# Kernel optimization log

Measured on AMD Instinct MI355X. Metric: run time of the kernel, lower is better.

## Reference

```python
import jax, jax.numpy as jnp
import numpy as np

WIN = 7
K1, K2 = 0.01, 0.03
NP_ = WIN ** 3
COV_NORM = NP_ / (NP_ - 1)


def _box3d(x, win=WIN):
    # Separable box filter: three 1D VALID convs (same math as the dense
    for ax in range(3):
        kshape = [1, 1, 1, 1, 1]
        kshape[2 + ax] = win
        k = jnp.ones(kshape, x.dtype) / win
        x = jax.lax.conv_general_dilated(
            x, k, window_strides=(1, 1, 1), padding='VALID',
            dimension_numbers=('NCDHW', 'OIDHW', 'NCDHW'))
    return x


def setup_inputs() -> dict:
    key = jax.random.key(0)
    k1, k2 = jax.random.split(key)
    B, C, D, H, W = 4, 1, 128, 128, 128
    X = jax.random.normal(k1, (B, C, D, H, W), dtype=jnp.float32)
    Y = jax.random.normal(k2, (B, C, D, H, W), dtype=jnp.float32)
    data_range = jnp.ones((B, 1, 1, 1, 1), dtype=jnp.float32)
    return {"X": X, "Y": Y, "data_range": data_range}


def reference(X, Y, data_range):
    C1 = (K1 * data_range) ** 2
    C2 = (K2 * data_range) ** 2
    ux = _box3d(X)
    uy = _box3d(Y)
    uxx = _box3d(X * X)
    uyy = _box3d(Y * Y)
    uxy = _box3d(X * Y)
    vx = COV_NORM * (uxx - ux * ux)
    vy = COV_NORM * (uyy - uy * uy)
    vxy = COV_NORM * (uxy - ux * uy)
    A1 = 2 * ux * uy + C1
    A2 = 2 * vxy + C2
    B1 = ux ** 2 + uy ** 2 + C1
    B2 = vx + vy + C2
    S = (A1 * A2) / (B1 * B2)
    return S.mean()
```

## Files before the change

### kernel.cpp

```cpp
#include <hip/hip_runtime.h>

#define NFULL 128
#define NOUT  122
#define NBLK  768

#define WROW 34
#define WQ   748
#define WB   3740
#define HROW 34
#define HQ   544
#define HB   2720

__device__ __forceinline__ void phaseA_task(const float* __restrict__ px,
                                            const float* __restrict__ py,
                                            float* __restrict__ wp)
{
    float xs[8], ys[8];
#pragma unroll
    for (int k = 0; k < 4; ++k) {
        float2 tx = *(const float2*)(px + 2 * k);
        float2 ty = *(const float2*)(py + 2 * k);
        xs[2 * k] = tx.x; xs[2 * k + 1] = tx.y;
        ys[2 * k] = ty.x; ys[2 * k + 1] = ty.y;
    }
    float sx = 0.f, sy = 0.f, sxx = 0.f, syy = 0.f, sxy = 0.f;
#pragma unroll
    for (int k = 0; k < 7; ++k) {
        sx += xs[k]; sy += ys[k];
        sxx = fmaf(xs[k], xs[k], sxx);
        syy = fmaf(ys[k], ys[k], syy);
        sxy = fmaf(xs[k], ys[k], sxy);
    }
    float tx2 = sx - xs[0] + xs[7];
    float ty2 = sy - ys[0] + ys[7];
    float txx = sxx - xs[0] * xs[0] + xs[7] * xs[7];
    float tyy = syy - ys[0] * ys[0] + ys[7] * ys[7];
    float txy = sxy - xs[0] * ys[0] + xs[7] * ys[7];
    *(float2*)(wp + 0 * WQ) = make_float2(sx,  tx2);
    *(float2*)(wp + 1 * WQ) = make_float2(sy,  ty2);
    *(float2*)(wp + 2 * WQ) = make_float2(sxx, txx);
    *(float2*)(wp + 3 * WQ) = make_float2(syy, tyy);
    *(float2*)(wp + 4 * WQ) = make_float2(sxy, txy);
}

__global__ __launch_bounds__(256, 3)
void ssim3d_kernel(const float* __restrict__ X, const float* __restrict__ Y,
                   const float* __restrict__ DR, double* __restrict__ ws,
                   float* __restrict__ out, int mode)
{
    __shared__ __align__(16) float wbuf[2 * WB];
    __shared__ __align__(16) float hbuf[2 * HB];
    __shared__ float  redf[4];
    __shared__ double redd[4];
    __shared__ int lastFlag;

    const int tid = threadIdx.x;
    int bi = blockIdx.x;
    const int bb = bi & 3;  bi >>= 2;
    const int ht = bi & 7;  bi >>= 3;
    const int wt = bi & 3;  bi >>= 2;
    const int dc = bi;

    const int h0 = ht << 4;
    const int w0 = (wt == 3) ? 90 : (wt << 5);
    const int w_hi = (wt == 3) ? 122 : ((wt == 2) ? 90 : (w0 + 32));
    const int csize = (dc < 2) ? 21 : 20;
    const int d0 = (dc < 2) ? dc * 21 : 42 + (dc - 2) * 20;
    const int nsl = csize + 6;

    const float dr = DR[bb];
    const float c1s = (0.01f * dr) * (0.01f * dr) * 117649.0f;
    const float c2s = (0.03f * dr) * (0.03f * dr) * 117649.0f;
    const float tni = 1.0f / 343.0f;
    const float kkA = 2.0f * 117649.0f / 342.0f;
    const float kkB = 117649.0f / 342.0f;

    const int sA  = tid & 15;
    const int rA0 = tid >> 4;
    int grA0 = h0 + rA0; if (grA0 > NFULL - 1) grA0 = NFULL - 1;
    const int coffA = w0 + 2 * sA;
    const int eA = tid - 192;
    int rA1 = 0, cA1 = 0, grA1 = 0, rA2 = 0, cA2 = 0, grA2 = 0;
    if (eA >= 0) {
        rA1 = 16 + (eA >> 4); cA1 = eA & 15;
        grA1 = h0 + rA1; if (grA1 > NFULL - 1) grA1 = NFULL - 1;
        if (eA < 32) {
            const int t = eA + 64;
            rA2 = 16 + (t >> 4); cA2 = t & 15;
            grA2 = h0 + rA2; if (grA2 > NFULL - 1) grA2 = NFULL - 1;
        }
    }

    const int bq = tid >> 5;
    const int bc = tid & 31;

    const int sC = tid & 15, hC = tid >> 4;
    const int gh  = h0 + hC;
    const int gw0 = w0 + 2 * sC;
    const bool vh = (gh < NOUT);
    const bool vld0 = vh && (gw0 < w_hi);
    const bool vld1 = vh && (gw0 + 1 < w_hi);

    const size_t planeStride = (size_t)NFULL * NFULL;
    const size_t bbase = (size_t)bb * NFULL * planeStride;

    float2 ring[7][5];
    float2 run[5];
#pragma unroll
    for (int k = 0; k < 7; ++k)
#pragma unroll
        for (int q = 0; q < 5; ++q) ring[k][q] = make_float2(0.f, 0.f);
#pragma unroll
    for (int q = 0; q < 5; ++q) run[q] = make_float2(0.f, 0.f);
    float acc = 0.0f;

    for (int base = 0; base <= nsl + 1; base += 7) {
#pragma unroll
        for (int u = 0; u < 7; ++u) {
            const int s = base + u;
            if (s <= nsl + 1) {
                if (s < nsl) {
                    float* dst = wbuf + (size_t)((s & 1) * WB);
                    const int dIn = d0 + s;
                    const float* Xp = X + bbase + (size_t)dIn * planeStride;
                    const float* Yp = Y + bbase + (size_t)dIn * planeStride;
                    phaseA_task(Xp + grA0 * NFULL + coffA, Yp + grA0 * NFULL + coffA,
                                dst + rA0 * WROW + 2 * sA);
                    if (eA >= 0) {
                        const int co1 = w0 + 2 * cA1;
                        phaseA_task(Xp + grA1 * NFULL + co1, Yp + grA1 * NFULL + co1,
                                    dst + rA1 * WROW + 2 * cA1);
                        if (eA < 32) {
                            const int co2 = w0 + 2 * cA2;
                            phaseA_task(Xp + grA2 * NFULL + co2, Yp + grA2 * NFULL + co2,
                                        dst + rA2 * WROW + 2 * cA2);
                        }
                    }
                }
                if (s >= 1 && tid < 160) {
                    const float* src = wbuf + (size_t)(((s - 1) & 1) * WB) + bq * WQ + bc;
                    float* dst = hbuf + (size_t)(((s - 1) & 1) * HB) + bq * HQ + bc;
                    float win = src[0] + src[WROW] + src[2 * WROW] + src[3 * WROW]
                              + src[4 * WROW] + src[5 * WROW];
#pragma unroll
                    for (int h = 0; h < 16; ++h) {
                        win += src[(h + 6) * WROW];
                        dst[h * HROW] = win;
                        win -= src[h * WROW];
                    }
                }
                if (s >= 2) {
                    const float* src = hbuf + (size_t)((s & 1) * HB) + hC * HROW + 2 * sC;
                    const int slot = (u + 5) % 7;
#pragma unroll
                    for (int q = 0; q < 5; ++q) {
                        float2 h2 = *(const float2*)(src + q * HQ);
                        run[q].x += h2.x - ring[slot][q].x;
                        run[q].y += h2.y - ring[slot][q].y;
                        ring[slot][q] = h2;
                    }
                    if (s >= 8) {
#pragma unroll
                        for (int j = 0; j < 2; ++j) {
                            const bool vld = j ? vld1 : vld0;
                            if (vld) {
                                float Sx  = j ? run[0].y : run[0].x;
                                float Sy  = j ? run[1].y : run[1].x;
                                float Sxx = j ? run[2].y : run[2].x;
                                float Syy = j ? run[3].y : run[3].x;
                                float Sxy = j ? run[4].y : run[4].x;
                                float P = Sx * Sy;
                                float Q = fmaf(Sx, Sx, Sy * Sy);
                                float A1 = fmaf(2.f, P, c1s);
                                float A2 = fmaf(kkA, fmaf(-tni, P, Sxy), c2s);
                                float B1 = Q + c1s;
                                float B2 = fmaf(kkB, fmaf(-tni, Q, Sxx + Syy), c2s);
                                float num = A1 * A2;
                                float den = B1 * B2;
                                float r0 = __builtin_amdgcn_rcpf(den);
                                r0 = r0 * fmaf(-den, r0, 2.0f);
                                acc = fmaf(num, r0, acc);
                            }
                        }
                    }
                }
                __syncthreads();
            }
        }
    }

#pragma unroll
    for (int off = 32; off; off >>= 1) acc += __shfl_down(acc, off);
    if ((tid & 63) == 0) redf[tid >> 6] = acc;
    __syncthreads();

    if (mode) {
        if (tid == 0) {
            double t = (double)redf[0] + (double)redf[1] + (double)redf[2] + (double)redf[3];
            ws[blockIdx.x] = t;
            __threadfence();
            unsigned int old = atomicAdd((unsigned int*)(ws + NBLK), 1u);
            lastFlag = (old == NBLK - 1) ? 1 : 0;
        }
        __syncthreads();
        if (lastFlag) {
            __threadfence();
            double t = 0.0;
            for (int i = tid; i < NBLK; i += 256) t += ws[i];
#pragma unroll
            for (int off = 32; off; off >>= 1) t += __shfl_down(t, off);
            if ((tid & 63) == 0) redd[tid >> 6] = t;
            __syncthreads();
            if (tid == 0)
                out[0] = (float)((redd[0] + redd[1] + redd[2] + redd[3])
                                 * (1.0 / 7263392.0));
        }
    } else {
        if (tid == 0) {
            double t = (double)redf[0] + (double)redf[1] + (double)redf[2] + (double)redf[3];
            atomicAdd(ws, t);
        }
    }
}

__global__ void ssim3d_finalize(const double* __restrict__ ws, float* __restrict__ out)
{
    out[0] = (float)(ws[0] * (1.0 / 7263392.0));
}

extern "C" void kernel_launch(void* const* d_in, const int* in_sizes, int n_in,
                              void* d_out, int out_size, void* d_ws, size_t ws_size,
                              hipStream_t stream)
{
    const float* X  = (const float*)d_in[0];
    const float* Y  = (const float*)d_in[1];
    const float* DR = (const float*)d_in[2];
    double* ws = (double*)d_ws;

    const int mode = (ws_size >= (size_t)(NBLK + 1) * sizeof(double)) ? 1 : 0;
    if (mode)
        hipMemsetAsync((char*)d_ws + (size_t)NBLK * sizeof(double), 0, sizeof(double), stream);
    else
        hipMemsetAsync(d_ws, 0, sizeof(double), stream);

    ssim3d_kernel<<<NBLK, 256, 0, stream>>>(X, Y, DR, ws, (float*)d_out, mode);
    if (!mode) ssim3d_finalize<<<1, 1, 0, stream>>>(ws, (float*)d_out);
}
```

Before: 146.3 us.

## Use 512-thread blocks with specialized warps and single-buffered staging

Blocks grow to 512 threads and the grid shrinks to 512 blocks, with larger depth chunks (30-31 slices) so each block re-reads fewer halo slices. Threads 160+ now load and do the W-pass while all threads do a one-pixel-per-thread depth ring and SSIM evaluation. Double buffering is replaced by single buffers with two barriers per slice. The aim is to cut halo reloads and raise parallelism, at the cost of more synchronization and a serialized H-pass phase.

```diff
diff --git a/kernel.cpp b/kernel.cpp
--- a/kernel.cpp
+++ b/kernel.cpp
@@ -2,7 +2,8 @@
 
 #define NFULL 128
 #define NOUT  122
-#define NBLK  768
+#define NBLK  512
+#define NTHR  512
 
 #define WROW 34
 #define WQ   748
@@ -43,15 +44,15 @@
     *(float2*)(wp + 4 * WQ) = make_float2(sxy, txy);
 }
 
-__global__ __launch_bounds__(256, 3)
+__global__ __launch_bounds__(NTHR, 4)
 void ssim3d_kernel(const float* __restrict__ X, const float* __restrict__ Y,
                    const float* __restrict__ DR, double* __restrict__ ws,
                    float* __restrict__ out, int mode)
 {
-    __shared__ __align__(16) float wbuf[2 * WB];
-    __shared__ __align__(16) float hbuf[2 * HB];
-    __shared__ float  redf[4];
-    __shared__ double redd[4];
+    __shared__ __align__(16) float wbuf[WB];
+    __shared__ __align__(16) float hbuf[HB];
+    __shared__ float  redf[8];
+    __shared__ double redd[8];
     __shared__ int lastFlag;
 
     const int tid = threadIdx.x;
@@ -64,8 +65,8 @@
     const int h0 = ht << 4;
     const int w0 = (wt == 3) ? 90 : (wt << 5);
     const int w_hi = (wt == 3) ? 122 : ((wt == 2) ? 90 : (w0 + 32));
-    const int csize = (dc < 2) ? 21 : 20;
-    const int d0 = (dc < 2) ? dc * 21 : 42 + (dc - 2) * 20;
+    const int csize = (dc < 2) ? 31 : 30;
+    const int d0 = (dc < 2) ? dc * 31 : 62 + (dc - 2) * 30;
     const int nsl = csize + 6;
 
     const float dr = DR[bb];
@@ -75,113 +76,84 @@
     const float kkA = 2.0f * 117649.0f / 342.0f;
     const float kkB = 117649.0f / 342.0f;
 
-    const int sA  = tid & 15;
-    const int rA0 = tid >> 4;
-    int grA0 = h0 + rA0; if (grA0 > NFULL - 1) grA0 = NFULL - 1;
+    const int aid = tid - 160;
+    const int rA  = aid >> 4;
+    const int sA  = aid & 15;
+    int grA = h0 + rA; if (grA > NFULL - 1) grA = NFULL - 1;
     const int coffA = w0 + 2 * sA;
-    const int eA = tid - 192;
-    int rA1 = 0, cA1 = 0, grA1 = 0, rA2 = 0, cA2 = 0, grA2 = 0;
-    if (eA >= 0) {
-        rA1 = 16 + (eA >> 4); cA1 = eA & 15;
-        grA1 = h0 + rA1; if (grA1 > NFULL - 1) grA1 = NFULL - 1;
-        if (eA < 32) {
-            const int t = eA + 64;
-            rA2 = 16 + (t >> 4); cA2 = t & 15;
-            grA2 = h0 + rA2; if (grA2 > NFULL - 1) grA2 = NFULL - 1;
-        }
-    }
 
     const int bq = tid >> 5;
     const int bc = tid & 31;
 
-    const int sC = tid & 15, hC = tid >> 4;
-    const int gh  = h0 + hC;
-    const int gw0 = w0 + 2 * sC;
-    const bool vh = (gh < NOUT);
-    const bool vld0 = vh && (gw0 < w_hi);
-    const bool vld1 = vh && (gw0 + 1 < w_hi);
+    const int sC = tid & 31, hC = tid >> 5;
+    const int gh = h0 + hC;
+    const int gw = w0 + sC;
+    const bool vld = (gh < NOUT) && (gw < w_hi);
 
     const size_t planeStride = (size_t)NFULL * NFULL;
     const size_t bbase = (size_t)bb * NFULL * planeStride;
 
-    float2 ring[7][5];
-    float2 run[5];
+    float ring[7][5];
+    float run[5];
 #pragma unroll
     for (int k = 0; k < 7; ++k)
 #pragma unroll
-        for (int q = 0; q < 5; ++q) ring[k][q] = make_float2(0.f, 0.f);
-#pragma unroll
-    for (int q = 0; q < 5; ++q) run[q] = make_float2(0.f, 0.f);
+        for (int q = 0; q < 5; ++q) ring[k][q] = 0.f;
+#pragma unroll
+    for (int q = 0; q < 5; ++q) run[q] = 0.f;
     float acc = 0.0f;
 
-    for (int base = 0; base <= nsl + 1; base += 7) {
+    for (int base = 0; base <= nsl; base += 7) {
 #pragma unroll
         for (int u = 0; u < 7; ++u) {
             const int s = base + u;
-            if (s <= nsl + 1) {
-                if (s < nsl) {
-                    float* dst = wbuf + (size_t)((s & 1) * WB);
+            if (s <= nsl) {
+                if (s < nsl && aid >= 0) {
                     const int dIn = d0 + s;
                     const float* Xp = X + bbase + (size_t)dIn * planeStride;
                     const float* Yp = Y + bbase + (size_t)dIn * planeStride;
-                    phaseA_task(Xp + grA0 * NFULL + coffA, Yp + grA0 * NFULL + coffA,
-                                dst + rA0 * WROW + 2 * sA);
-                    if (eA >= 0) {
-                        const int co1 = w0 + 2 * cA1;
-                        phaseA_task(Xp + grA1 * NFULL + co1, Yp + grA1 * NFULL + co1,
-                                    dst + rA1 * WROW + 2 * cA1);
-                        if (eA < 32) {
-                            const int co2 = w0 + 2 * cA2;
-                            phaseA_task(Xp + grA2 * NFULL + co2, Yp + grA2 * NFULL + co2,
-                                        dst + rA2 * WROW + 2 * cA2);
-                        }
+                    phaseA_task(Xp + grA * NFULL + coffA, Yp + grA * NFULL + coffA,
+                                wbuf + rA * WROW + 2 * sA);
+                }
+                if (s >= 1) {
+                    const float* src = hbuf + hC * HROW + sC;
+                    const int slot = (u + 6) % 7;
+#pragma unroll
+                    for (int q = 0; q < 5; ++q) {
+                        float v = src[q * HQ];
+                        run[q] += v - ring[slot][q];
+                        ring[slot][q] = v;
+                    }
+                    if (s >= 7 && vld) {
+                        float Sx  = run[0];
+                        float Sy  = run[1];
+                        float Sxx = run[2];
+                        float Syy = run[3];
+                        float Sxy = run[4];
+                        float P = Sx * Sy;
+                        float Q = fmaf(Sx, Sx, Sy * Sy);
+                        float A1 = fmaf(2.f, P, c1s);
+                        float A2 = fmaf(kkA, fmaf(-tni, P, Sxy), c2s);
+                        float B1 = Q + c1s;
+                        float B2 = fmaf(kkB, fmaf(-tni, Q, Sxx + Syy), c2s);
+                        float num = A1 * A2;
+                        float den = B1 * B2;
+                        float r0 = __builtin_amdgcn_rcpf(den);
+                        r0 = r0 * fmaf(-den, r0, 2.0f);
+                        acc = fmaf(num, r0, acc);
                     }
                 }
-                if (s >= 1 && tid < 160) {
-                    const float* src = wbuf + (size_t)(((s - 1) & 1) * WB) + bq * WQ + bc;
-                    float* dst = hbuf + (size_t)(((s - 1) & 1) * HB) + bq * HQ + bc;
-                    float win = src[0] + src[WROW] + src[2 * WROW] + src[3 * WROW]
-                              + src[4 * WROW] + src[5 * WROW];
+                __syncthreads();
+                if (s < nsl && tid < 160) {
+                    const float* srcw = wbuf + bq * WQ + bc;
+                    float* dsth = hbuf + bq * HQ + bc;
+                    float win = srcw[0] + srcw[WROW] + srcw[2 * WROW]
+                              + srcw[3 * WROW] + srcw[4 * WROW] + srcw[5 * WROW];
 #pragma unroll
                     for (int h = 0; h < 16; ++h) {
-                        win += src[(h + 6) * WROW];
-                        dst[h * HROW] = win;
-                        win -= src[h * WROW];
-                    }
-                }
-                if (s >= 2) {
-                    const float* src = hbuf + (size_t)((s & 1) * HB) + hC * HROW + 2 * sC;
-                    const int slot = (u + 5) % 7;
-#pragma unroll
-                    for (int q = 0; q < 5; ++q) {
-                        float2 h2 = *(const float2*)(src + q * HQ);
-                        run[q].x += h2.x - ring[slot][q].x;
-                        run[q].y += h2.y - ring[slot][q].y;
-                        ring[slot][q] = h2;
-                    }
-                    if (s >= 8) {
-#pragma unroll
-                        for (int j = 0; j < 2; ++j) {
-                            const bool vld = j ? vld1 : vld0;
-                            if (vld) {
-                                float Sx  = j ? run[0].y : run[0].x;
-                                float Sy  = j ? run[1].y : run[1].x;
-                                float Sxx = j ? run[2].y : run[2].x;
-                                float Syy = j ? run[3].y : run[3].x;
-                                float Sxy = j ? run[4].y : run[4].x;
-                                float P = Sx * Sy;
-                                float Q = fmaf(Sx, Sx, Sy * Sy);
-                                float A1 = fmaf(2.f, P, c1s);
-                                float A2 = fmaf(kkA, fmaf(-tni, P, Sxy), c2s);
-                                float B1 = Q + c1s;
-                                float B2 = fmaf(kkB, fmaf(-tni, Q, Sxx + Syy), c2s);
-                                float num = A1 * A2;
-                                float den = B1 * B2;
-                                float r0 = __builtin_amdgcn_rcpf(den);
-                                r0 = r0 * fmaf(-den, r0, 2.0f);
-                                acc = fmaf(num, r0, acc);
-                            }
-                        }
+                        win += srcw[(h + 6) * WROW];
+                        dsth[h * HROW] = win;
+                        win -= srcw[h * WROW];
                     }
                 }
                 __syncthreads();
@@ -196,7 +168,9 @@
 
     if (mode) {
         if (tid == 0) {
-            double t = (double)redf[0] + (double)redf[1] + (double)redf[2] + (double)redf[3];
+            double t = 0.0;
+#pragma unroll
+            for (int i = 0; i < 8; ++i) t += (double)redf[i];
             ws[blockIdx.x] = t;
             __threadfence();
             unsigned int old = atomicAdd((unsigned int*)(ws + NBLK), 1u);
@@ -206,18 +180,23 @@
         if (lastFlag) {
             __threadfence();
             double t = 0.0;
-            for (int i = tid; i < NBLK; i += 256) t += ws[i];
+            for (int i = tid; i < NBLK; i += NTHR) t += ws[i];
 #pragma unroll
             for (int off = 32; off; off >>= 1) t += __shfl_down(t, off);
             if ((tid & 63) == 0) redd[tid >> 6] = t;
             __syncthreads();
-            if (tid == 0)
-                out[0] = (float)((redd[0] + redd[1] + redd[2] + redd[3])
-                                 * (1.0 / 7263392.0));
+            if (tid == 0) {
+                double r = 0.0;
+#pragma unroll
+                for (int i = 0; i < 8; ++i) r += redd[i];
+                out[0] = (float)(r * (1.0 / 7263392.0));
+            }
         }
     } else {
         if (tid == 0) {
-            double t = (double)redf[0] + (double)redf[1] + (double)redf[2] + (double)redf[3];
+            double t = 0.0;
+#pragma unroll
+            for (int i = 0; i < 8; ++i) t += (double)redf[i];
             atomicAdd(ws, t);
         }
     }
@@ -243,6 +222,6 @@
     else
         hipMemsetAsync(d_ws, 0, sizeof(double), stream);
 
-    ssim3d_kernel<<<NBLK, 256, 0, stream>>>(X, Y, DR, ws, (float*)d_out, mode);
+    ssim3d_kernel<<<NBLK, NTHR, 0, stream>>>(X, Y, DR, ws, (float*)d_out, mode);
     if (!mode) ssim3d_finalize<<<1, 1, 0, stream>>>(ws, (float*)d_out);
 }
```

Measured after the change: 142.2 us. 1.03x faster.
